# Performance work log

Measured on AMD Instinct MI355X. Metric: run time of the kernel, lower is better.

Reference implementation:

```python
import jax, jax.numpy as jnp
import numpy as np

EMB = 1024
HEADS = 16
HD = EMB // HEADS
EPS = 1e-5

def _ln(x, g, b):
    m = jnp.mean(x, axis=-1, keepdims=True)
    v = jnp.mean((x - m) ** 2, axis=-1, keepdims=True)
    return (x - m) * jax.lax.rsqrt(v + EPS) * g + b

def setup_inputs() -> dict:
    key = jax.random.key(0)
    ks = jax.random.split(key, 12)
    s_in = 1.0 / np.sqrt(EMB)
    s_ff = 1.0 / np.sqrt(4 * EMB)
    return {
        "x": jax.random.normal(ks[0], (2, 2048, EMB), jnp.float32),
        "wq": jax.random.uniform(ks[1], (HEADS, EMB, HD), jnp.float32, -s_in, s_in),
        "wk": jax.random.uniform(ks[2], (HEADS, EMB, HD), jnp.float32, -s_in, s_in),
        "wv": jax.random.uniform(ks[3], (HEADS, EMB, HD), jnp.float32, -s_in, s_in),
        "wo": jax.random.uniform(ks[4], (EMB, EMB), jnp.float32, -s_in, s_in),
        "bo": jax.random.uniform(ks[5], (EMB,), jnp.float32, -s_in, s_in),
        "g1": jnp.ones((EMB,), jnp.float32),
        "b1": jnp.zeros((EMB,), jnp.float32),
        "g2": jnp.ones((EMB,), jnp.float32),
        "b2": jnp.zeros((EMB,), jnp.float32),
        "w1": jax.random.uniform(ks[6], (EMB, 4 * EMB), jnp.float32, -s_in, s_in),
        "bf1": jax.random.uniform(ks[7], (4 * EMB,), jnp.float32, -s_in, s_in),
        "w2": jax.random.uniform(ks[8], (4 * EMB, EMB), jnp.float32, -s_ff, s_ff),
        "bf2": jax.random.uniform(ks[9], (EMB,), jnp.float32, -s_ff, s_ff),
    }

def reference(x, wq, wk, wv, wo, bo, g1, b1, g2, b2, w1, bf1, w2, bf2):
    B, T, C = x.shape
    h = _ln(x, g1, b1)
    # all heads batched: [B,H,T,HD]
    q = jnp.einsum('btc,hcd->bhtd', h, wq)
    k = jnp.einsum('btc,hcd->bhtd', h, wk)
    v = jnp.einsum('btc,hcd->bhtd', h, wv)
    # NOTE: original scales by full emb_size C**-0.5, not head_size
    scores = jnp.einsum('bhtd,bhsd->bhts', q, k) * (C ** -0.5)
    causal = jnp.tril(jnp.ones((T, T), bool))
    scores = jnp.where(causal, scores, -jnp.inf)
    w = jax.nn.softmax(scores, axis=-1)
    attn = jnp.einsum('bhts,bhsd->bhtd', w, v)
    attn = attn.transpose(0, 2, 1, 3).reshape(B, T, C)  # concat heads
    x = x + attn @ wo + bo
    h2 = _ln(x, g2, b2)
    ffn = jax.nn.relu(h2 @ w1 + bf1) @ w2 + bf2
    return x + ffn
```

## Files before the change

kernel.cpp:

```cpp
#include <hip/hip_runtime.h>

typedef __bf16 bf16x8 __attribute__((ext_vector_type(8)));
typedef float f32x4 __attribute__((ext_vector_type(4)));
typedef short s16x8 __attribute__((ext_vector_type(8)));

#define DEV __device__ __forceinline__

DEV float b2f(unsigned short u) {
  unsigned int x = ((unsigned int)u) << 16;
  return __builtin_bit_cast(float, x);
}
DEV unsigned short f2b(float f) {
  unsigned int x = __builtin_bit_cast(unsigned int, f);
  x += 0x7fffu + ((x >> 16) & 1u);
  return (unsigned short)(x >> 16);
}
DEV f32x4 mfma16(bf16x8 a, bf16x8 b, f32x4 c) {
  return __builtin_amdgcn_mfma_f32_16x16x32_bf16(a, b, c, 0, 0, 0);
}
DEV void gl2lds16(const unsigned short* g, unsigned short* l) {
  __builtin_amdgcn_global_load_lds(
      (const __attribute__((address_space(1))) void*)g,
      (__attribute__((address_space(3))) void*)l, 16, 0, 0);
}

__global__ __launch_bounds__(256)
void transpose_k(const float* __restrict__ in, unsigned short* __restrict__ out,
                 int K, int N, long zin, long zout) {
  __shared__ float tile[32][33];
  in  += (size_t)blockIdx.z * zin;
  out += (size_t)blockIdx.z * zout;
  int n0 = blockIdx.x * 32, k0 = blockIdx.y * 32;
  int tx = threadIdx.x, ty = threadIdx.y;
  #pragma unroll
  for (int i = ty; i < 32; i += 8)
    tile[i][tx] = in[(size_t)(k0 + i) * N + n0 + tx];
  __syncthreads();
  #pragma unroll
  for (int i = ty; i < 32; i += 8)
    out[(size_t)(n0 + i) * K + k0 + tx] = f2b(tile[tx][i]);
}

__global__ __launch_bounds__(256)
void vtrans_k(const unsigned short* __restrict__ qkv, unsigned short* __restrict__ vT) {
  __shared__ unsigned short tile[32][33];
  int bh = blockIdx.z, b = bh >> 4, h = bh & 15;
  int t0 = blockIdx.x * 32, d0 = blockIdx.y * 32;
  const unsigned short* in = qkv + (size_t)b * 2048 * 3072 + 2048 + h * 64;
  unsigned short* out = vT + (size_t)bh * 64 * 2048;
  int tx = threadIdx.x, ty = threadIdx.y;
  #pragma unroll
  for (int i = ty; i < 32; i += 8)
    tile[i][tx] = in[(size_t)(t0 + i) * 3072 + d0 + tx];
  __syncthreads();
  #pragma unroll
  for (int i = ty; i < 32; i += 8)
    out[(size_t)(d0 + i) * 2048 + t0 + tx] = tile[tx][i];
}

__global__ __launch_bounds__(256)
void ln_kernel(const float* __restrict__ x, const float* __restrict__ g,
               const float* __restrict__ b, unsigned short* __restrict__ o) {
  __shared__ float rs[4];
  __shared__ float rq[4];
  int row = blockIdx.x, tid = threadIdx.x;
  const float* xr = x + (size_t)row * 1024;
  float4 raw = ((const float4*)xr)[tid];
  float s = raw.x + raw.y + raw.z + raw.w;
  float q = raw.x*raw.x + raw.y*raw.y + raw.z*raw.z + raw.w*raw.w;
  #pragma unroll
  for (int off = 32; off > 0; off >>= 1) {
    s += __shfl_down(s, off);
    q += __shfl_down(q, off);
  }
  int wave = tid >> 6;
  if ((tid & 63) == 0) { rs[wave] = s; rq[wave] = q; }
  __syncthreads();
  float ts = rs[0] + rs[1] + rs[2] + rs[3];
  float tq = rq[0] + rq[1] + rq[2] + rq[3];
  float mean = ts * (1.0f/1024.0f);
  float var = tq * (1.0f/1024.0f) - mean*mean;
  float rstd = rsqrtf(var + 1e-5f);
  float4 gr = ((const float4*)g)[tid];
  float4 br = ((const float4*)b)[tid];
  float o0 = (raw.x-mean)*rstd*gr.x + br.x;
  float o1 = (raw.y-mean)*rstd*gr.y + br.y;
  float o2 = (raw.z-mean)*rstd*gr.z + br.z;
  float o3 = (raw.w-mean)*rstd*gr.w + br.w;
  uint2 ov;
  ov.x = (unsigned int)f2b(o0) | ((unsigned int)f2b(o1) << 16);
  ov.y = (unsigned int)f2b(o2) | ((unsigned int)f2b(o3) << 16);
  ((uint2*)(o + (size_t)row * 1024))[tid] = ov;
}

template<bool RELU, bool BIAS, bool RESID, bool OUTF32>
__global__ __launch_bounds__(256)
void gemm_bt(const unsigned short* __restrict__ A, const unsigned short* __restrict__ Bt,
             const float* __restrict__ bias, const float* __restrict__ resid,
             void* __restrict__ Cv, int M, int N, int K) {
  __shared__ unsigned short As[2][128*32];
  __shared__ unsigned short Bs[2][128*32];
  const int tid = threadIdx.x;
  const int lane = tid & 63;
  const int quad = lane >> 4, l16 = lane & 15;
  const int wave = tid >> 6;
  const int m0 = blockIdx.y * 128, n0 = blockIdx.x * 128;
  const int wm = (wave >> 1) * 64, wn = (wave & 1) * 64;

  f32x4 acc[4][4];
  #pragma unroll
  for (int i = 0; i < 4; ++i)
    #pragma unroll
    for (int j = 0; j < 4; ++j) acc[i][j] = (f32x4){0.f, 0.f, 0.f, 0.f};

  const int srow = tid >> 2;
  const int scol = (tid & 3) * 8;
  const unsigned short* Ab = A + (size_t)m0 * K;
  const unsigned short* Bb = Bt + (size_t)n0 * K;

  auto stage = [&](int buf, int k0) {
    gl2lds16(Ab + (size_t)srow * K + k0 + scol,        &As[buf][tid * 8]);
    gl2lds16(Ab + (size_t)(srow + 64) * K + k0 + scol, &As[buf][2048 + tid * 8]);
    gl2lds16(Bb + (size_t)srow * K + k0 + scol,        &Bs[buf][tid * 8]);
    gl2lds16(Bb + (size_t)(srow + 64) * K + k0 + scol, &Bs[buf][2048 + tid * 8]);
  };

  const int niter = K >> 5;
  stage(0, 0);
  __syncthreads();

  for (int it = 0; it < niter; ++it) {
    const int buf = it & 1;
    if (it + 1 < niter) stage(buf ^ 1, (it + 1) * 32);
    bf16x8 af[4], bfr[4];
    #pragma unroll
    for (int i = 0; i < 4; ++i)
      af[i] = __builtin_bit_cast(bf16x8, *(const s16x8*)&As[buf][(wm + i*16 + l16)*32 + quad*8]);
    #pragma unroll
    for (int j = 0; j < 4; ++j)
      bfr[j] = __builtin_bit_cast(bf16x8, *(const s16x8*)&Bs[buf][(wn + j*16 + l16)*32 + quad*8]);
    #pragma unroll
    for (int i = 0; i < 4; ++i)
      #pragma unroll
      for (int j = 0; j < 4; ++j)
        acc[i][j] = mfma16(af[i], bfr[j], acc[i][j]);
    __syncthreads();
  }

  #pragma unroll
  for (int i = 0; i < 4; ++i) {
    const int row = m0 + wm + i*16 + quad*4;
    #pragma unroll
    for (int j = 0; j < 4; ++j) {
      const int col = n0 + wn + j*16 + l16;
      float bv = 0.f;
      if (BIAS) bv = bias[col];
      #pragma unroll
      for (int r = 0; r < 4; ++r) {
        float v = acc[i][j][r] + bv;
        if (RESID) v += resid[(size_t)(row + r) * N + col];
        if (RELU) v = fmaxf(v, 0.f);
        if (OUTF32) ((float*)Cv)[(size_t)(row + r) * N + col] = v;
        else ((unsigned short*)Cv)[(size_t)(row + r) * N + col] = f2b(v);
      }
    }
  }
}

__global__ __launch_bounds__(256)
void gemm_bt64(const unsigned short* __restrict__ A, const unsigned short* __restrict__ Bt,
               const float* __restrict__ bias, const float* __restrict__ resid,
               float* __restrict__ C, int M, int N, int K) {
  __shared__ unsigned short As[2][64*32];
  __shared__ unsigned short Bs[2][128*32];
  const int tid = threadIdx.x;
  const int lane = tid & 63;
  const int quad = lane >> 4, l16 = lane & 15;
  const int wave = tid >> 6;
  const int id = blockIdx.x;
  const int xcd = id & 7, i2 = id >> 3;
  const int mt = (xcd << 3) | (i2 >> 3);
  const int nt = i2 & 7;
  const int m0 = mt * 64, n0 = nt * 128;
  const int wm = (wave >> 1) * 32, wn = (wave & 1) * 64;

  f32x4 acc[2][4];
  #pragma unroll
  for (int i = 0; i < 2; ++i)
    #pragma unroll
    for (int j = 0; j < 4; ++j) acc[i][j] = (f32x4){0.f, 0.f, 0.f, 0.f};

  const int srow = tid >> 2;
  const int scol = (tid & 3) * 8;
  const unsigned short* Ab = A + (size_t)m0 * K;
  const unsigned short* Bb = Bt + (size_t)n0 * K;

  auto stage = [&](int buf, int k0) {
    gl2lds16(Ab + (size_t)srow * K + k0 + scol,        &As[buf][tid * 8]);
    gl2lds16(Bb + (size_t)srow * K + k0 + scol,        &Bs[buf][tid * 8]);
    gl2lds16(Bb + (size_t)(srow + 64) * K + k0 + scol, &Bs[buf][2048 + tid * 8]);
  };

  const int niter = K >> 5;
  stage(0, 0);
  __syncthreads();

  for (int it = 0; it < niter; ++it) {
    const int buf = it & 1;
    if (it + 1 < niter) stage(buf ^ 1, (it + 1) * 32);
    bf16x8 af[2], bfr[4];
    #pragma unroll
    for (int i = 0; i < 2; ++i)
      af[i] = __builtin_bit_cast(bf16x8, *(const s16x8*)&As[buf][(wm + i*16 + l16)*32 + quad*8]);
    #pragma unroll
    for (int j = 0; j < 4; ++j)
      bfr[j] = __builtin_bit_cast(bf16x8, *(const s16x8*)&Bs[buf][(wn + j*16 + l16)*32 + quad*8]);
    #pragma unroll
    for (int i = 0; i < 2; ++i)
      #pragma unroll
      for (int j = 0; j < 4; ++j)
        acc[i][j] = mfma16(af[i], bfr[j], acc[i][j]);
    __syncthreads();
  }

  #pragma unroll
  for (int i = 0; i < 2; ++i) {
    const int row = m0 + wm + i*16 + quad*4;
    #pragma unroll
    for (int j = 0; j < 4; ++j) {
      const int col = n0 + wn + j*16 + l16;
      const float bv = bias[col];
      #pragma unroll
      for (int r = 0; r < 4; ++r) {
        float v = acc[i][j][r] + bv + resid[(size_t)(row + r) * N + col];
        C[(size_t)(row + r) * N + col] = v;
      }
    }
  }
}

__global__ __launch_bounds__(256)
void attn_kernel(const unsigned short* __restrict__ qkv,
                 const unsigned short* __restrict__ vT,
                 unsigned short* __restrict__ outc) {
  __shared__ unsigned short Ks[2][64*64];
  __shared__ unsigned short Vs[2][64*64];
  __shared__ unsigned short Ps[2][4*16*72];
  const int tid = threadIdx.x, lane = tid & 63, wave = tid >> 6;
  const int quad = lane >> 4, l16 = lane & 15;
  const int bh = blockIdx.y, b = bh >> 4, h = bh & 15;
  const int jA = blockIdx.x, jB = 31 - jA;
  const size_t tokbase = (size_t)b * 2048 * 3072;
  const unsigned short* Q  = qkv + tokbase + h * 64;
  const unsigned short* Kg = qkv + tokbase + 1024 + h * 64;
  const unsigned short* Vg = vT + (size_t)bh * 64 * 2048;

  bf16x8 qf[2][2];
  #pragma unroll
  for (int t = 0; t < 2; ++t) {
    const int qrow = (t ? jB : jA) * 64 + wave * 16 + l16;
    #pragma unroll
    for (int s = 0; s < 2; ++s) {
      s16x8 raw = *(const s16x8*)(Q + (size_t)qrow * 3072 + s * 32 + quad * 8);
      unsigned short* rp = (unsigned short*)&raw;
      #pragma unroll
      for (int j = 0; j < 8; ++j) rp[j] = f2b(b2f(rp[j]) * 0.03125f);
      qf[t][s] = __builtin_bit_cast(bf16x8, raw);
    }
  }

  f32x4 accO[2][4];
  #pragma unroll
  for (int t = 0; t < 2; ++t)
    #pragma unroll
    for (int i = 0; i < 4; ++i) accO[t][i] = (f32x4){0.f, 0.f, 0.f, 0.f};
  float lrow[2][4] = {{0.f,0.f,0.f,0.f},{0.f,0.f,0.f,0.f}};

  const int r8 = lane >> 3;
  const int cs = (((lane & 7) ^ r8) * 8);

  auto stage = [&](int buf, int kv0) {
    #pragma unroll
    for (int i = 0; i < 2; ++i) {
      int row = wave * 16 + i * 8;
      gl2lds16(Kg + (size_t)(kv0 + row + r8) * 3072 + cs, &Ks[buf][row * 64 + lane * 8]);
      gl2lds16(Vg + (size_t)(row + r8) * 2048 + kv0 + cs, &Vs[buf][row * 64 + lane * 8]);
    }
  };

  const int ntile = jB + 1;
  stage(0, 0);
  __syncthreads();

  for (int it = 0; it < ntile; ++it) {
    const int buf = it & 1;
    if (it + 1 < ntile) stage(buf ^ 1, (it + 1) * 64);

    #pragma unroll
    for (int t = 0; t < 2; ++t) {
      const int jT = t ? jB : jA;
      if (it > jT) continue;
      f32x4 sv[4];
      #pragma unroll
      for (int ni = 0; ni < 4; ++ni) {
        sv[ni] = (f32x4){0.f, 0.f, 0.f, 0.f};
        #pragma unroll
        for (int s = 0; s < 2; ++s) {
          bf16x8 kf = __builtin_bit_cast(bf16x8,
            *(const s16x8*)&Ks[buf][(ni*16 + l16)*64 + (((s*4 + quad) ^ (l16 & 7)) * 8)]);
          sv[ni] = mfma16(qf[t][s], kf, sv[ni]);
        }
      }
      if (it == jT) {
        const int rowg = jT*64 + wave*16 + quad*4;
        const int kv0 = it * 64;
        #pragma unroll
        for (int ni = 0; ni < 4; ++ni) {
          const int colg = kv0 + ni*16 + l16;
          #pragma unroll
          for (int r = 0; r < 4; ++r)
            if (colg > rowg + r) sv[ni][r] = -__builtin_inff();
        }
      }
      float rsum[4] = {0.f, 0.f, 0.f, 0.f};
      unsigned short pb[4][4];
      #pragma unroll
      for (int ni = 0; ni < 4; ++ni)
        #pragma unroll
        for (int r = 0; r < 4; ++r) {
          float p = __expf(sv[ni][r]);
          rsum[r] += p;
          pb[ni][r] = f2b(p);
        }
      #pragma unroll
      for (int r = 0; r < 4; ++r) {
        float s2 = rsum[r];
        s2 += __shfl_xor(s2, 1);
        s2 += __shfl_xor(s2, 2);
        s2 += __shfl_xor(s2, 4);
        s2 += __shfl_xor(s2, 8);
        lrow[t][r] += s2;
      }
      #pragma unroll
      for (int ni = 0; ni < 4; ++ni)
        #pragma unroll
        for (int r = 0; r < 4; ++r)
          Ps[t][wave*1152 + (quad*4 + r)*72 + ni*16 + l16] = pb[ni][r];
      __asm__ volatile("s_waitcnt lgkmcnt(0)" ::: "memory");
      #pragma unroll
      for (int s = 0; s < 2; ++s) {
        bf16x8 pf = __builtin_bit_cast(bf16x8,
          *(const s16x8*)&Ps[t][wave*1152 + l16*72 + s*32 + quad*8]);
        #pragma unroll
        for (int ni = 0; ni < 4; ++ni) {
          bf16x8 vf = __builtin_bit_cast(bf16x8,
            *(const s16x8*)&Vs[buf][(ni*16 + l16)*64 + (((s*4 + quad) ^ (l16 & 7)) * 8)]);
          accO[t][ni] = mfma16(pf, vf, accO[t][ni]);
        }
      }
    }
    __syncthreads();
  }

  #pragma unroll
  for (int t = 0; t < 2; ++t) {
    const int rowg = (t ? jB : jA)*64 + wave*16 + quad*4;
    #pragma unroll
    for (int ni = 0; ni < 4; ++ni)
      #pragma unroll
      for (int r = 0; r < 4; ++r) {
        float o = accO[t][ni][r] / lrow[t][r];
        outc[(size_t)(b*2048 + rowg + r) * 1024 + h*64 + ni*16 + l16] = f2b(o);
      }
  }
}

extern "C" void kernel_launch(void* const* d_in, const int* in_sizes, int n_in,
                              void* d_out, int out_size, void* d_ws, size_t ws_size,
                              hipStream_t stream) {
  (void)in_sizes; (void)n_in; (void)out_size; (void)ws_size;
  const float* x   = (const float*)d_in[0];
  const float* wq  = (const float*)d_in[1];
  const float* wk  = (const float*)d_in[2];
  const float* wv  = (const float*)d_in[3];
  const float* wo  = (const float*)d_in[4];
  const float* bo  = (const float*)d_in[5];
  const float* g1  = (const float*)d_in[6];
  const float* b1  = (const float*)d_in[7];
  const float* g2  = (const float*)d_in[8];
  const float* b2  = (const float*)d_in[9];
  const float* w1  = (const float*)d_in[10];
  const float* bf1 = (const float*)d_in[11];
  const float* w2  = (const float*)d_in[12];
  const float* bf2 = (const float*)d_in[13];
  float* out = (float*)d_out;

  unsigned short* ws    = (unsigned short*)d_ws;
  unsigned short* wqkvt = ws;
  unsigned short* wot   = wqkvt + 3*1024*1024;
  unsigned short* w1t   = wot   + 1024*1024;
  unsigned short* w2t   = w1t   + 4096*1024;
  unsigned short* hbuf  = w2t   + 4096*1024;
  unsigned short* qkvb  = hbuf  + 4096*1024;
  unsigned short* attnb = qkvb  + (size_t)4096*3072;
  float*          x2b   = (float*)(attnb + 4096*1024);
  unsigned short* vTb   = (unsigned short*)x2b;
  unsigned short* midb  = qkvb;

  dim3 tb(32, 8);
  transpose_k<<<dim3(2,32,16), tb, 0, stream>>>(wq, wqkvt,             1024, 64, 65536, 65536);
  transpose_k<<<dim3(2,32,16), tb, 0, stream>>>(wk, wqkvt + 1024*1024, 1024, 64, 65536, 65536);
  transpose_k<<<dim3(2,32,16), tb, 0, stream>>>(wv, wqkvt + 2048*1024, 1024, 64, 65536, 65536);
  transpose_k<<<dim3(32,32,1),  tb, 0, stream>>>(wo, wot, 1024, 1024, 0, 0);
  transpose_k<<<dim3(128,32,1), tb, 0, stream>>>(w1, w1t, 1024, 4096, 0, 0);
  transpose_k<<<dim3(32,128,1), tb, 0, stream>>>(w2, w2t, 4096, 1024, 0, 0);

  ln_kernel<<<4096, 256, 0, stream>>>(x, g1, b1, hbuf);
  gemm_bt<false,false,false,false><<<dim3(24,32), 256, 0, stream>>>(hbuf, wqkvt, nullptr, nullptr, qkvb, 4096, 3072, 1024);
  vtrans_k<<<dim3(64,2,32), tb, 0, stream>>>(qkvb, vTb);
  attn_kernel<<<dim3(16,32), 256, 0, stream>>>(qkvb, vTb, attnb);
  gemm_bt64<<<512, 256, 0, stream>>>(attnb, wot, bo, x, x2b, 4096, 1024, 1024);
  ln_kernel<<<4096, 256, 0, stream>>>(x2b, g2, b2, hbuf);
  gemm_bt<true,true,false,false><<<dim3(32,32), 256, 0, stream>>>(hbuf, w1t, bf1, nullptr, midb, 4096, 4096, 1024);
  gemm_bt64<<<512, 256, 0, stream>>>(midb, w2t, bf2, x2b, out, 4096, 1024, 4096);
}
```

Measured before the change: 380.6 us.

## Use 128x128 tiles with triple-buffered LDS pipeline in N=1024 GEMMs

```diff
diff --git a/kernel.cpp b/kernel.cpp
--- a/kernel.cpp
+++ b/kernel.cpp
@@ -168,25 +168,25 @@
 }
 
 __global__ __launch_bounds__(256)
-void gemm_bt64(const unsigned short* __restrict__ A, const unsigned short* __restrict__ Bt,
+void gemm_pipe(const unsigned short* __restrict__ A, const unsigned short* __restrict__ Bt,
                const float* __restrict__ bias, const float* __restrict__ resid,
                float* __restrict__ C, int M, int N, int K) {
-  __shared__ unsigned short As[2][64*32];
-  __shared__ unsigned short Bs[2][128*32];
+  __shared__ unsigned short As[3][128*32];
+  __shared__ unsigned short Bs[3][128*32];
   const int tid = threadIdx.x;
   const int lane = tid & 63;
   const int quad = lane >> 4, l16 = lane & 15;
   const int wave = tid >> 6;
   const int id = blockIdx.x;
   const int xcd = id & 7, i2 = id >> 3;
-  const int mt = (xcd << 3) | (i2 >> 3);
-  const int nt = i2 & 7;
-  const int m0 = mt * 64, n0 = nt * 128;
-  const int wm = (wave >> 1) * 32, wn = (wave & 1) * 64;
-
-  f32x4 acc[2][4];
-  #pragma unroll
-  for (int i = 0; i < 2; ++i)
+  const int mt = (xcd << 2) | (i2 & 3);
+  const int nt = i2 >> 2;
+  const int m0 = mt * 128, n0 = nt * 128;
+  const int wm = (wave >> 1) * 64, wn = (wave & 1) * 64;
+
+  f32x4 acc[4][4];
+  #pragma unroll
+  for (int i = 0; i < 4; ++i)
     #pragma unroll
     for (int j = 0; j < 4; ++j) acc[i][j] = (f32x4){0.f, 0.f, 0.f, 0.f};
 
@@ -197,44 +197,54 @@
 
   auto stage = [&](int buf, int k0) {
     gl2lds16(Ab + (size_t)srow * K + k0 + scol,        &As[buf][tid * 8]);
+    gl2lds16(Ab + (size_t)(srow + 64) * K + k0 + scol, &As[buf][2048 + tid * 8]);
     gl2lds16(Bb + (size_t)srow * K + k0 + scol,        &Bs[buf][tid * 8]);
     gl2lds16(Bb + (size_t)(srow + 64) * K + k0 + scol, &Bs[buf][2048 + tid * 8]);
   };
 
   const int niter = K >> 5;
   stage(0, 0);
-  __syncthreads();
-
+  stage(1, 32);
+
+  int buf = 0;
   for (int it = 0; it < niter; ++it) {
-    const int buf = it & 1;
-    if (it + 1 < niter) stage(buf ^ 1, (it + 1) * 32);
-    bf16x8 af[2], bfr[4];
-    #pragma unroll
-    for (int i = 0; i < 2; ++i)
+    if (it + 2 < niter) {
+      const int nbuf = (buf == 0) ? 2 : buf - 1;
+      stage(nbuf, (it + 2) * 32);
+      __asm__ volatile("s_waitcnt vmcnt(8)\ns_barrier" ::: "memory");
+    } else if (it + 1 < niter) {
+      __asm__ volatile("s_waitcnt vmcnt(4)\ns_barrier" ::: "memory");
+    } else {
+      __asm__ volatile("s_waitcnt vmcnt(0)\ns_barrier" ::: "memory");
+    }
+
+    bf16x8 af[4], bfr[4];
+    #pragma unroll
+    for (int i = 0; i < 4; ++i)
       af[i] = __builtin_bit_cast(bf16x8, *(const s16x8*)&As[buf][(wm + i*16 + l16)*32 + quad*8]);
     #pragma unroll
     for (int j = 0; j < 4; ++j)
       bfr[j] = __builtin_bit_cast(bf16x8, *(const s16x8*)&Bs[buf][(wn + j*16 + l16)*32 + quad*8]);
     #pragma unroll
-    for (int i = 0; i < 2; ++i)
+    for (int i = 0; i < 4; ++i)
       #pragma unroll
       for (int j = 0; j < 4; ++j)
         acc[i][j] = mfma16(af[i], bfr[j], acc[i][j]);
-    __syncthreads();
-  }
-
-  #pragma unroll
-  for (int i = 0; i < 2; ++i) {
+
+    __asm__ volatile("s_barrier" ::: "memory");
+    buf = (buf == 2) ? 0 : buf + 1;
+  }
+
+  #pragma unroll
+  for (int i = 0; i < 4; ++i) {
     const int row = m0 + wm + i*16 + quad*4;
     #pragma unroll
     for (int j = 0; j < 4; ++j) {
       const int col = n0 + wn + j*16 + l16;
       const float bv = bias[col];
       #pragma unroll
-      for (int r = 0; r < 4; ++r) {
-        float v = acc[i][j][r] + bv + resid[(size_t)(row + r) * N + col];
-        C[(size_t)(row + r) * N + col] = v;
-      }
+      for (int r = 0; r < 4; ++r)
+        C[(size_t)(row + r) * N + col] = acc[i][j][r] + bv + resid[(size_t)(row + r) * N + col];
     }
   }
 }
@@ -419,8 +429,8 @@
   gemm_bt<false,false,false,false><<<dim3(24,32), 256, 0, stream>>>(hbuf, wqkvt, nullptr, nullptr, qkvb, 4096, 3072, 1024);
   vtrans_k<<<dim3(64,2,32), tb, 0, stream>>>(qkvb, vTb);
   attn_kernel<<<dim3(16,32), 256, 0, stream>>>(qkvb, vTb, attnb);
-  gemm_bt64<<<512, 256, 0, stream>>>(attnb, wot, bo, x, x2b, 4096, 1024, 1024);
+  gemm_pipe<<<256, 256, 0, stream>>>(attnb, wot, bo, x, x2b, 4096, 1024, 1024);
   ln_kernel<<<4096, 256, 0, stream>>>(x2b, g2, b2, hbuf);
   gemm_bt<true,true,false,false><<<dim3(32,32), 256, 0, stream>>>(hbuf, w1t, bf1, nullptr, midb, 4096, 4096, 1024);
-  gemm_bt64<<<512, 256, 0, stream>>>(midb, w2t, bf2, x2b, out, 4096, 1024, 4096);
-}
+  gemm_pipe<<<256, 256, 0, stream>>>(midb, w2t, bf2, x2b, out, 4096, 1024, 4096);
+}
```

After: 394.5 us. +3.7%, slower.
